# Kernel tuning notes

Hardware: AMD Instinct MI355X
Metric: run time of the kernel (lower is better)

## Reference

```python
import jax, jax.numpy as jnp
import numpy as np

N_NODES = 50000
N_EDGES = 1600000
IN_DIM = 128
HID = 64
N_GRAPHS = 256


def gcn_conv(x, row, col, W, b, n_nodes):
    """PyG GCNConv: symmetric gcn_norm with self-loops, linear-then-aggregate."""
    h = x @ W  # [N, out]
    loop = jnp.arange(n_nodes, dtype=row.dtype)
    r = jnp.concatenate([row, loop])  # sources (messages from x[r])
    c = jnp.concatenate([col, loop])  # targets (aggregate at c)
    ew = jnp.ones(r.shape[0], dtype=x.dtype)
    deg = jax.ops.segment_sum(ew, c, num_segments=n_nodes)
    dinv = jnp.where(deg > 0, jax.lax.rsqrt(deg), 0.0).astype(x.dtype)
    norm = dinv[r] * dinv[c]  # [E+N]
    out = jax.ops.segment_sum(norm[:, None] * h[r], c, num_segments=n_nodes)
    return out + b


def global_mean_pool(x, batch, n_graphs):
    sums = jax.ops.segment_sum(x, batch, num_segments=n_graphs)
    cnt = jax.ops.segment_sum(jnp.ones(x.shape[0], x.dtype), batch, num_segments=n_graphs)
    return sums / jnp.clip(cnt, 1.0)[:, None]


def setup_inputs() -> dict:
    key = jax.random.key(0)
    ks = jax.random.split(key, 12)
    x = jax.random.normal(ks[0], (N_NODES, IN_DIM), dtype=jnp.float32)
    edge_index = jax.random.randint(ks[1], (2, N_EDGES), 0, N_NODES, dtype=jnp.int64)
    batch = jnp.sort(jax.random.randint(ks[2], (N_NODES,), 0, N_GRAPHS, dtype=jnp.int64))
    def glorot(k, shp):
        lim = float(np.sqrt(6.0 / (shp[0] + shp[1])))
        return jax.random.uniform(k, shp, jnp.float32, -lim, lim)
    return {
        "x": x,
        "edge_index": edge_index,
        "batch": batch,
        "W1": glorot(ks[3], (IN_DIM, HID)), "b1": jnp.zeros((HID,), jnp.float32),
        "W2": glorot(ks[4], (HID, HID)), "b2": jnp.zeros((HID,), jnp.float32),
        "W3": glorot(ks[5], (HID, HID)), "b3": jnp.zeros((HID,), jnp.float32),
        "Wl1": glorot(ks[6], (HID, 16)), "bl1": jnp.zeros((16,), jnp.float32),
        "Wl2": glorot(ks[7], (16, 1)), "bl2": jnp.zeros((1,), jnp.float32),
    }


def reference(x, edge_index, batch, W1, b1, W2, b2, W3, b3, Wl1, bl1, Wl2, bl2):
    n = x.shape[0]
    row, col = edge_index[0], edge_index[1]
    h = jax.nn.relu(gcn_conv(x, row, col, W1, b1, n))
    h = jax.nn.relu(gcn_conv(h, row, col, W2, b2, n))
    h = jax.nn.relu(gcn_conv(h, row, col, W3, b3, n))
    g = global_mean_pool(h, batch, N_GRAPHS)  # [G, 64]
    out = (g @ Wl1 + bl1) @ Wl2 + bl2  # [G, 1]
    return out
```

## Files before the change

### kernel.cpp

```cpp
#include <hip/hip_runtime.h>

#define HID 64
#define B1 512
#define NBMAX 200
#define CAP 10368
#define ENTCAP 3456

typedef __attribute__((ext_vector_type(8))) short short8;
typedef __attribute__((ext_vector_type(4))) float float4v;

__device__ __forceinline__ ushort f2bf(float f) {
  unsigned u = __float_as_uint(f);
  unsigned r = (u + 0x7fffu + ((u >> 16) & 1u)) >> 16;
  return (ushort)r;
}
__device__ __forceinline__ float bf2f(ushort v) {
  return __uint_as_float(((unsigned)v) << 16);
}
__device__ __forceinline__ float4 up4(ushort4 v) {
  float4 r;
  r.x = bf2f(v.x);
  r.y = bf2f(v.y);
  r.z = bf2f(v.z);
  r.w = bf2f(v.w);
  return r;
}


__global__ __launch_bounds__(256) void bucket_hist(const int* __restrict__ col, int E, int epb,
                                                   int* __restrict__ blockcnt,
                                                   const float* __restrict__ W1,
                                                   const float* __restrict__ W2,
                                                   const float* __restrict__ W3,
                                                   ushort* __restrict__ Wt1h, ushort* __restrict__ Wt1l,
                                                   ushort* __restrict__ Wt2h, ushort* __restrict__ Wt2l,
                                                   ushort* __restrict__ Wt3h, ushort* __restrict__ Wt3l) {
  int b = blockIdx.x, t = threadIdx.x;
  int gt = b * 256 + t;
  if (gt < 128 * 64) {
    int k = gt >> 6, nn = gt & 63;
    float w = W1[gt];
    ushort h = f2bf(w);
    Wt1h[nn * 128 + k] = h;
    Wt1l[nn * 128 + k] = f2bf(w - bf2f(h));
  }
  if (gt < 64 * 64) {
    int k = gt >> 6, nn = gt & 63;
    float w2 = W2[gt], w3 = W3[gt];
    ushort h2 = f2bf(w2), h3 = f2bf(w3);
    Wt2h[nn * 64 + k] = h2;
    Wt2l[nn * 64 + k] = f2bf(w2 - bf2f(h2));
    Wt3h[nn * 64 + k] = h3;
    Wt3l[nn * 64 + k] = f2bf(w3 - bf2f(h3));
  }

  __shared__ int cnt[256];
  cnt[t] = 0;
  __syncthreads();
  int lo = b * epb, hi = min(lo + epb, E);
  for (int e = lo + t; e < hi; e += 256) atomicAdd(&cnt[col[e] >> 8], 1);
  __syncthreads();
  blockcnt[b * 256 + t] = cnt[t];
}

__global__ __launch_bounds__(512) void scan_blocks(int* __restrict__ blockcnt,
                                                   int* __restrict__ buckettot) {
  __shared__ int s[512];
  int k = blockIdx.x;
  int t = threadIdx.x;
  int v = blockcnt[t * 256 + k];
  s[t] = v;
  __syncthreads();
  for (int d = 1; d < 512; d <<= 1) {
    int u = (t >= d) ? s[t - d] : 0;
    __syncthreads();
    s[t] += u;
    __syncthreads();
  }
  blockcnt[t * 256 + k] = s[t] - v;
  if (t == 511) buckettot[k] = s[t];
}

__global__ __launch_bounds__(256) void scan_buckettot(const int* __restrict__ buckettot,
                                                      int* __restrict__ bucketbase,
                                                      int* __restrict__ csr_off, int n, int E,
                                                      int nb) {
  __shared__ int s[256];
  int t = threadIdx.x;
  int v = buckettot[t];
  s[t] = v;
  __syncthreads();
  for (int d = 1; d < 256; d <<= 1) {
    int u = (t >= d) ? s[t - d] : 0;
    __syncthreads();
    s[t] += u;
    __syncthreads();
  }
  bucketbase[t] = s[t] - v;
  if (t == 255) bucketbase[256] = s[255];
  if (t == 0) csr_off[n] = E;
}

__global__ __launch_bounds__(256) void bin_edges(const int* __restrict__ row,
                                                 const int* __restrict__ col, int E, int epb,
                                                 const int* __restrict__ blockcnt,
                                                 const int* __restrict__ bucketbase,
                                                 unsigned* __restrict__ binned) {
  __shared__ int cnt[256];
  __shared__ int ofs[256];
  __shared__ int gb[256];
  __shared__ int lcur[256];
  __shared__ unsigned ent[ENTCAP];
  __shared__ unsigned stage[ENTCAP];
  int b = blockIdx.x, t = threadIdx.x;
  int lo = b * epb, hi = min(lo + epb, E);
  int ecnt = hi - lo;

  cnt[t] = 0;
  __syncthreads();
  for (int i = t; i < ecnt; i += 256) {
    int c = col[lo + i];
    int r = row[lo + i];
    ent[i] = ((unsigned)r << 16) | (unsigned)c;
    atomicAdd(&cnt[c >> 8], 1);
  }
  __syncthreads();
  int v = cnt[t];
  ofs[t] = v;
  __syncthreads();
  for (int d = 1; d < 256; d <<= 1) {
    int u = (t >= d) ? ofs[t - d] : 0;
    __syncthreads();
    ofs[t] += u;
    __syncthreads();
  }
  int excl = ofs[t] - v;
  int g = bucketbase[t] + blockcnt[b * 256 + t];
  __syncthreads();
  ofs[t] = excl;
  gb[t] = g;
  lcur[t] = excl;
  __syncthreads();
  for (int i = t; i < ecnt; i += 256) {
    unsigned en = ent[i];
    int p = atomicAdd(&lcur[(en >> 8) & 255], 1);
    stage[p] = en;
  }
  __syncthreads();
  for (int i = t; i < ecnt; i += 256) {
    unsigned en = stage[i];
    int bb = (en >> 8) & 255;
    binned[gb[bb] + (i - ofs[bb])] = en;
  }
}

__global__ __launch_bounds__(512) void bucket_csr(const unsigned* __restrict__ binned,
                                                  const int* __restrict__ bucketbase,
                                                  int* __restrict__ csr_off,
                                                  int* __restrict__ csr_src,
                                                  float* __restrict__ dinv, int n) {
  __shared__ int lcnt[256];
  __shared__ int lofs[256];
  __shared__ int lsrc[CAP];
  int k = blockIdx.x, t = threadIdx.x;
  int base = bucketbase[k], end = bucketbase[k + 1];
  int s = end - base;
  if (t < 256) lcnt[t] = 0;
  __syncthreads();
  for (int i = t; i < s; i += 512) {
    unsigned p = binned[base + i];
    atomicAdd(&lcnt[p & 255u], 1);
  }
  __syncthreads();
  int v = 0;
  if (t < 256) {
    v = lcnt[t];
    lofs[t] = v;
  }
  __syncthreads();
  for (int d = 1; d < 256; d <<= 1) {
    int u = (t < 256 && t >= d) ? lofs[t - d] : 0;
    __syncthreads();
    if (t < 256) lofs[t] += u;
    __syncthreads();
  }
  if (t < 256) {
    int excl = lofs[t] - v;
    int node = (k << 8) + t;
    if (node < n) {
      csr_off[node] = base + excl;
      dinv[node] = rsqrtf((float)(v + 1));
    }
    lcnt[t] = excl;
  }
  __syncthreads();
  for (int i = t; i < s; i += 512) {
    unsigned p = binned[base + i];
    int pos = atomicAdd(&lcnt[p & 255u], 1);
    if (pos < CAP) lsrc[pos] = (int)(p >> 16);
  }
  __syncthreads();
  for (int i = t; i < s; i += 512) csr_src[base + i] = (i < CAP) ? lsrc[i] : 0;
}


template <int K>
__global__ __launch_bounds__(256) void gemm_mfma(const float* __restrict__ A,
                                                 const ushort* __restrict__ Wh,
                                                 const ushort* __restrict__ Wl,
                                                 const float* __restrict__ dinv,
                                                 ushort* __restrict__ out, int n) {
  int wave = (blockIdx.x * 256 + threadIdx.x) >> 6;
  int lane = threadIdx.x & 63;
  int row0 = wave * 16;
  if (row0 >= n) return;
  int m = lane & 15;
  int quad = lane >> 4;
  int r = row0 + m;
  int rc = (r < n) ? r : (n - 1);

  float4v acc[4];
#pragma unroll
  for (int t = 0; t < 4; ++t) acc[t] = (float4v){0.f, 0.f, 0.f, 0.f};

#pragma unroll
  for (int k0 = 0; k0 < K; k0 += 32) {
    const float4* xp = (const float4*)&A[(size_t)rc * K + k0 + quad * 8];
    float4 a0 = xp[0];
    float4 a1 = xp[1];
    float av[8] = {a0.x, a0.y, a0.z, a0.w, a1.x, a1.y, a1.z, a1.w};
    short8 ah, al;
#pragma unroll
    for (int i = 0; i < 8; ++i) {
      ushort h = f2bf(av[i]);
      ah[i] = (short)h;
      al[i] = (short)f2bf(av[i] - bf2f(h));
    }
#pragma unroll
    for (int t = 0; t < 4; ++t) {
      size_t wof = (size_t)(t * 16 + m) * K + k0 + quad * 8;
      short8 bh = *(const short8*)&Wh[wof];
      short8 bl = *(const short8*)&Wl[wof];
      acc[t] = __builtin_amdgcn_mfma_f32_16x16x32_bf16(ah, bh, acc[t], 0, 0, 0);
      acc[t] = __builtin_amdgcn_mfma_f32_16x16x32_bf16(al, bh, acc[t], 0, 0, 0);
      acc[t] = __builtin_amdgcn_mfma_f32_16x16x32_bf16(ah, bl, acc[t], 0, 0, 0);
    }
  }

  float4 dv = ((const float4*)dinv)[(row0 >> 2) + quad];
  float dvi[4] = {dv.x, dv.y, dv.z, dv.w};
#pragma unroll
  for (int i = 0; i < 4; ++i) {
    int orow = row0 + quad * 4 + i;
    if (orow < n) {
#pragma unroll
      for (int t = 0; t < 4; ++t) {
        out[(size_t)orow * 64 + t * 16 + m] = f2bf(dvi[i] * acc[t][i]);
      }
    }
  }
}


__global__ __launch_bounds__(256) void agg_kernel(
    const ushort* __restrict__ hs, const int* __restrict__ csr_off,
    const int* __restrict__ csr_src, const float* __restrict__ dinv,
    const float* __restrict__ bias, float* __restrict__ out, int n) {
  int wid = (blockIdx.x * 256 + threadIdx.x) >> 6;
  int lane = threadIdx.x & 63;
  if (wid >= n) return;
  int qe = lane >> 4;
  int fq = lane & 15;
  const ushort4* hs4 = (const ushort4*)hs;

  float4 acc = make_float4(0.f, 0.f, 0.f, 0.f);
  if (qe == 0) {
    float4 s = up4(hs4[(size_t)wid * 16 + fq]);
    acc.x += s.x; acc.y += s.y; acc.z += s.z; acc.w += s.w;
  }

  int j = csr_off[wid];
  int e = csr_off[wid + 1];

  int pre = min(e, (j + 3) & ~3);
  if (j + qe < pre) {
    int s0 = csr_src[j + qe];
    float4 f = up4(hs4[(size_t)s0 * 16 + fq]);
    acc.x += f.x; acc.y += f.y; acc.z += f.z; acc.w += f.w;
  }
  int base = pre;

  for (; base + 16 <= e; base += 16) {
    int4 s = *(const int4*)&csr_src[base + qe * 4];
    float4 f0 = up4(hs4[(size_t)s.x * 16 + fq]);
    float4 f1 = up4(hs4[(size_t)s.y * 16 + fq]);
    float4 f2 = up4(hs4[(size_t)s.z * 16 + fq]);
    float4 f3 = up4(hs4[(size_t)s.w * 16 + fq]);
    acc.x += f0.x + f1.x + f2.x + f3.x;
    acc.y += f0.y + f1.y + f2.y + f3.y;
    acc.z += f0.z + f1.z + f2.z + f3.z;
    acc.w += f0.w + f1.w + f2.w + f3.w;
  }

  for (; base + 4 <= e; base += 4) {
    int s0 = csr_src[base + qe];
    float4 f = up4(hs4[(size_t)s0 * 16 + fq]);
    acc.x += f.x; acc.y += f.y; acc.z += f.z; acc.w += f.w;
  }
  if (base + qe < e) {
    int s0 = csr_src[base + qe];
    float4 f = up4(hs4[(size_t)s0 * 16 + fq]);
    acc.x += f.x; acc.y += f.y; acc.z += f.z; acc.w += f.w;
  }

  acc.x += __shfl_xor(acc.x, 16, 64);
  acc.y += __shfl_xor(acc.y, 16, 64);
  acc.z += __shfl_xor(acc.z, 16, 64);
  acc.w += __shfl_xor(acc.w, 16, 64);
  acc.x += __shfl_xor(acc.x, 32, 64);
  acc.y += __shfl_xor(acc.y, 32, 64);
  acc.z += __shfl_xor(acc.z, 32, 64);
  acc.w += __shfl_xor(acc.w, 32, 64);

  if (qe == 0) {
    float d = dinv[wid];
    float4 bi = ((const float4*)bias)[fq];
    float4 r;
    r.x = fmaxf(d * acc.x + bi.x, 0.f);
    r.y = fmaxf(d * acc.y + bi.y, 0.f);
    r.z = fmaxf(d * acc.z + bi.z, 0.f);
    r.w = fmaxf(d * acc.w + bi.w, 0.f);
    ((float4*)out)[(size_t)wid * 16 + fq] = r;
  }
}


__global__ __launch_bounds__(256) void pool_mlp_kernel(
    const float* __restrict__ a, const int* __restrict__ batch, int n,
    const float* __restrict__ Wl1, const float* __restrict__ bl1,
    const float* __restrict__ Wl2, const float* __restrict__ bl2,
    float* __restrict__ out) {
  int g = blockIdx.x;
  int t = threadIdx.x;
  int lane = t & 63;
  int w = t >> 6;

  int lo = 0, hi = n;
  while (lo < hi) {
    int m = (lo + hi) >> 1;
    if (batch[m] < g) lo = m + 1; else hi = m;
  }
  int start = lo;
  lo = start; hi = n;
  while (lo < hi) {
    int m = (lo + hi) >> 1;
    if (batch[m] < g + 1) lo = m + 1; else hi = m;
  }
  int end = lo;

  float s = 0.f;
  for (int i = start + w; i < end; i += 4) s += a[i * 64 + lane];

  __shared__ float ps[4][64];
  __shared__ float gv[64];
  __shared__ float hv[16];
  ps[w][lane] = s;
  __syncthreads();
  if (w == 0) {
    float tot = ps[0][lane] + ps[1][lane] + ps[2][lane] + ps[3][lane];
    gv[lane] = tot / (float)max(end - start, 1);
  }
  __syncthreads();
  if (t < 16) {
    float h = bl1[t];
    for (int k = 0; k < 64; ++k) h += gv[k] * Wl1[k * 16 + t];
    hv[t] = h;
  }
  __syncthreads();
  if (t == 0) {
    float o = bl2[0];
    for (int j2 = 0; j2 < 16; ++j2) o += hv[j2] * Wl2[j2];
    out[g] = o;
  }
}


extern "C" void kernel_launch(void* const* d_in, const int* in_sizes, int n_in,
                              void* d_out, int out_size, void* d_ws, size_t ws_size,
                              hipStream_t stream) {
  const float* x = (const float*)d_in[0];
  const int* ei = (const int*)d_in[1];
  const int* batch = (const int*)d_in[2];
  const float* W1 = (const float*)d_in[3];
  const float* b1 = (const float*)d_in[4];
  const float* W2 = (const float*)d_in[5];
  const float* b2 = (const float*)d_in[6];
  const float* W3 = (const float*)d_in[7];
  const float* b3 = (const float*)d_in[8];
  const float* Wl1 = (const float*)d_in[9];
  const float* bl1 = (const float*)d_in[10];
  const float* Wl2 = (const float*)d_in[11];
  const float* bl2 = (const float*)d_in[12];

  int n = in_sizes[0] / 128;
  int E = in_sizes[1] / 2;
  int G = out_size;
  int nb = (n + 255) >> 8;
  int epb = (E + B1 - 1) / B1;

  const int* row = ei;
  const int* col = ei + E;

  char* p = (char*)d_ws;
  int* blockcnt = (int*)p;    p += B1 * 256 * 4;
  int* buckettot = (int*)p;   p += 256 * 4;
  int* bucketbase = (int*)p;  p += 272 * 4;
  int* csr_off = (int*)p;     p += 50064 * 4;
  float* dinv = (float*)p;    p += 50016 * 4;
  ushort* Wt1h = (ushort*)p;  p += 128 * 64 * 2;
  ushort* Wt1l = (ushort*)p;  p += 128 * 64 * 2;
  ushort* Wt2h = (ushort*)p;  p += 64 * 64 * 2;
  ushort* Wt2l = (ushort*)p;  p += 64 * 64 * 2;
  ushort* Wt3h = (ushort*)p;  p += 64 * 64 * 2;
  ushort* Wt3l = (ushort*)p;  p += 64 * 64 * 2;
  int* csr_src = (int*)p;     p += (size_t)((E + 15) / 16 * 16) * 4;
  ushort* hs = (ushort*)p;    p += (size_t)n * 64 * 2;
  float* abuf = (float*)p;
  unsigned* binned = (unsigned*)hs;

  bucket_hist<<<B1, 256, 0, stream>>>(col, E, epb, blockcnt,
                                      W1, W2, W3, Wt1h, Wt1l, Wt2h, Wt2l, Wt3h, Wt3l);
  scan_blocks<<<256, 512, 0, stream>>>(blockcnt, buckettot);
  scan_buckettot<<<1, 256, 0, stream>>>(buckettot, bucketbase, csr_off, n, E, nb);
  bin_edges<<<B1, 256, 0, stream>>>(row, col, E, epb, blockcnt, bucketbase, binned);
  bucket_csr<<<nb, 512, 0, stream>>>(binned, bucketbase, csr_off, csr_src, dinv, n);

  int nwaves = (n + 15) / 16;
  int gblocks = (nwaves + 3) / 4;
  int ablocks = (n * 64 + 255) / 256;

  gemm_mfma<128><<<gblocks, 256, 0, stream>>>(x, Wt1h, Wt1l, dinv, hs, n);
  agg_kernel<<<ablocks, 256, 0, stream>>>(hs, csr_off, csr_src, dinv, b1, abuf, n);
  gemm_mfma<64><<<gblocks, 256, 0, stream>>>(abuf, Wt2h, Wt2l, dinv, hs, n);
  agg_kernel<<<ablocks, 256, 0, stream>>>(hs, csr_off, csr_src, dinv, b2, abuf, n);
  gemm_mfma<64><<<gblocks, 256, 0, stream>>>(abuf, Wt3h, Wt3l, dinv, hs, n);
  agg_kernel<<<ablocks, 256, 0, stream>>>(hs, csr_off, csr_src, dinv, b3, abuf, n);
  pool_mlp_kernel<<<G, 256, 0, stream>>>(abuf, batch, n, Wl1, bl1, Wl2, bl2, (float*)d_out);
}
```

Measured before the change: 309.5 us.

## Vectorize edge loads, cache binned entries in registers, pack bf16 accumulation

The histogram and binning kernels now read col/row as int4 vectors, with epb rounded up to a multiple of 16 so each block's start stays aligned. bucket_csr keeps each thread's binned entries in a fixed register array so the second pass skips the global re-read. The aggregation kernel unpacks bf16 pairs with shifts and masks into packed float2 accumulators instead of four scalar converts. ENTCAP shrinks to match the new per-block edge count. The cost removed is extra global traffic and conversion ALU work, at the price of more registers and a hard cap of 21 entries per thread in bucket_csr; entries past that limit are never read, so correctness now depends on bucket sizes staying within the cap.

Result: no change. 306.9 us (-0.8%).

```diff
diff --git a/kernel.cpp b/kernel.cpp
--- a/kernel.cpp
+++ b/kernel.cpp
@@ -4,10 +4,12 @@
 #define B1 512
 #define NBMAX 200
 #define CAP 10368
-#define ENTCAP 3456
+#define ENTCAP 3200
+#define CPT 21
 
 typedef __attribute__((ext_vector_type(8))) short short8;
 typedef __attribute__((ext_vector_type(4))) float float4v;
+typedef float f32x2 __attribute__((ext_vector_type(2)));
 
 __device__ __forceinline__ ushort f2bf(float f) {
   unsigned u = __float_as_uint(f);
@@ -17,13 +19,15 @@
 __device__ __forceinline__ float bf2f(ushort v) {
   return __uint_as_float(((unsigned)v) << 16);
 }
-__device__ __forceinline__ float4 up4(ushort4 v) {
-  float4 r;
-  r.x = bf2f(v.x);
-  r.y = bf2f(v.y);
-  r.z = bf2f(v.z);
-  r.w = bf2f(v.w);
-  return r;
+
+__device__ __forceinline__ void acc8(f32x2& a01, f32x2& a23, uint2 d) {
+  f32x2 t0, t1;
+  t0.x = __uint_as_float(d.x << 16);
+  t0.y = __uint_as_float(d.x & 0xffff0000u);
+  t1.x = __uint_as_float(d.y << 16);
+  t1.y = __uint_as_float(d.y & 0xffff0000u);
+  a01 += t0;
+  a23 += t1;
 }
 
 
@@ -58,7 +62,18 @@
   cnt[t] = 0;
   __syncthreads();
   int lo = b * epb, hi = min(lo + epb, E);
-  for (int e = lo + t; e < hi; e += 256) atomicAdd(&cnt[col[e] >> 8], 1);
+  int ecnt = hi - lo;
+  if (ecnt > 0) {
+    int ecnt4 = ecnt & ~3;
+    for (int i = t * 4; i < ecnt4; i += 1024) {
+      int4 c4 = *(const int4*)&col[lo + i];
+      atomicAdd(&cnt[c4.x >> 8], 1);
+      atomicAdd(&cnt[c4.y >> 8], 1);
+      atomicAdd(&cnt[c4.z >> 8], 1);
+      atomicAdd(&cnt[c4.w >> 8], 1);
+    }
+    for (int i = ecnt4 + t; i < ecnt; i += 256) atomicAdd(&cnt[col[lo + i] >> 8], 1);
+  }
   __syncthreads();
   blockcnt[b * 256 + t] = cnt[t];
 }
@@ -118,11 +133,28 @@
 
   cnt[t] = 0;
   __syncthreads();
-  for (int i = t; i < ecnt; i += 256) {
-    int c = col[lo + i];
-    int r = row[lo + i];
-    ent[i] = ((unsigned)r << 16) | (unsigned)c;
-    atomicAdd(&cnt[c >> 8], 1);
+  if (ecnt > 0) {
+    int ecnt4 = ecnt & ~3;
+    for (int i = t * 4; i < ecnt4; i += 1024) {
+      int4 c4 = *(const int4*)&col[lo + i];
+      int4 r4 = *(const int4*)&row[lo + i];
+      uint4 e4;
+      e4.x = ((unsigned)r4.x << 16) | (unsigned)c4.x;
+      e4.y = ((unsigned)r4.y << 16) | (unsigned)c4.y;
+      e4.z = ((unsigned)r4.z << 16) | (unsigned)c4.z;
+      e4.w = ((unsigned)r4.w << 16) | (unsigned)c4.w;
+      *(uint4*)&ent[i] = e4;
+      atomicAdd(&cnt[c4.x >> 8], 1);
+      atomicAdd(&cnt[c4.y >> 8], 1);
+      atomicAdd(&cnt[c4.z >> 8], 1);
+      atomicAdd(&cnt[c4.w >> 8], 1);
+    }
+    for (int i = ecnt4 + t; i < ecnt; i += 256) {
+      int c = col[lo + i];
+      int r = row[lo + i];
+      ent[i] = ((unsigned)r << 16) | (unsigned)c;
+      atomicAdd(&cnt[c >> 8], 1);
+    }
   }
   __syncthreads();
   int v = cnt[t];
@@ -141,16 +173,20 @@
   gb[t] = g;
   lcur[t] = excl;
   __syncthreads();
-  for (int i = t; i < ecnt; i += 256) {
-    unsigned en = ent[i];
-    int p = atomicAdd(&lcur[(en >> 8) & 255], 1);
-    stage[p] = en;
-  }
-  __syncthreads();
-  for (int i = t; i < ecnt; i += 256) {
-    unsigned en = stage[i];
-    int bb = (en >> 8) & 255;
-    binned[gb[bb] + (i - ofs[bb])] = en;
+  if (ecnt > 0) {
+    for (int i = t; i < ecnt; i += 256) {
+      unsigned en = ent[i];
+      int p = atomicAdd(&lcur[(en >> 8) & 255], 1);
+      stage[p] = en;
+    }
+  }
+  __syncthreads();
+  if (ecnt > 0) {
+    for (int i = t; i < ecnt; i += 256) {
+      unsigned en = stage[i];
+      int bb = (en >> 8) & 255;
+      binned[gb[bb] + (i - ofs[bb])] = en;
+    }
   }
 }
 
@@ -165,11 +201,17 @@
   int k = blockIdx.x, t = threadIdx.x;
   int base = bucketbase[k], end = bucketbase[k + 1];
   int s = end - base;
+  unsigned ent[CPT];
   if (t < 256) lcnt[t] = 0;
   __syncthreads();
-  for (int i = t; i < s; i += 512) {
-    unsigned p = binned[base + i];
-    atomicAdd(&lcnt[p & 255u], 1);
+#pragma unroll
+  for (int q = 0; q < CPT; ++q) {
+    int i = q * 512 + t;
+    if (i < s) {
+      unsigned p = binned[base + i];
+      ent[q] = p;
+      atomicAdd(&lcnt[p & 255u], 1);
+    }
   }
   __syncthreads();
   int v = 0;
@@ -194,10 +236,14 @@
     lcnt[t] = excl;
   }
   __syncthreads();
-  for (int i = t; i < s; i += 512) {
-    unsigned p = binned[base + i];
-    int pos = atomicAdd(&lcnt[p & 255u], 1);
-    if (pos < CAP) lsrc[pos] = (int)(p >> 16);
+#pragma unroll
+  for (int q = 0; q < CPT; ++q) {
+    int i = q * 512 + t;
+    if (i < s) {
+      unsigned p = ent[q];
+      int pos = atomicAdd(&lcnt[p & 255u], 1);
+      if (pos < CAP) lsrc[pos] = (int)(p >> 16);
+    }
   }
   __syncthreads();
   for (int i = t; i < s; i += 512) csr_src[base + i] = (i < CAP) ? lsrc[i] : 0;
@@ -271,12 +317,11 @@
   if (wid >= n) return;
   int qe = lane >> 4;
   int fq = lane & 15;
-  const ushort4* hs4 = (const ushort4*)hs;
-
-  float4 acc = make_float4(0.f, 0.f, 0.f, 0.f);
+  const uint2* hs2 = (const uint2*)hs;
+
+  f32x2 a01 = {0.f, 0.f}, a23 = {0.f, 0.f};
   if (qe == 0) {
-    float4 s = up4(hs4[(size_t)wid * 16 + fq]);
-    acc.x += s.x; acc.y += s.y; acc.z += s.z; acc.w += s.w;
+    acc8(a01, a23, hs2[(size_t)wid * 16 + fq]);
   }
 
   int j = csr_off[wid];
@@ -285,51 +330,48 @@
   int pre = min(e, (j + 3) & ~3);
   if (j + qe < pre) {
     int s0 = csr_src[j + qe];
-    float4 f = up4(hs4[(size_t)s0 * 16 + fq]);
-    acc.x += f.x; acc.y += f.y; acc.z += f.z; acc.w += f.w;
+    acc8(a01, a23, hs2[(size_t)s0 * 16 + fq]);
   }
   int base = pre;
 
   for (; base + 16 <= e; base += 16) {
     int4 s = *(const int4*)&csr_src[base + qe * 4];
-    float4 f0 = up4(hs4[(size_t)s.x * 16 + fq]);
-    float4 f1 = up4(hs4[(size_t)s.y * 16 + fq]);
-    float4 f2 = up4(hs4[(size_t)s.z * 16 + fq]);
-    float4 f3 = up4(hs4[(size_t)s.w * 16 + fq]);
-    acc.x += f0.x + f1.x + f2.x + f3.x;
-    acc.y += f0.y + f1.y + f2.y + f3.y;
-    acc.z += f0.z + f1.z + f2.z + f3.z;
-    acc.w += f0.w + f1.w + f2.w + f3.w;
+    uint2 v0 = hs2[(size_t)s.x * 16 + fq];
+    uint2 v1 = hs2[(size_t)s.y * 16 + fq];
+    uint2 v2 = hs2[(size_t)s.z * 16 + fq];
+    uint2 v3 = hs2[(size_t)s.w * 16 + fq];
+    acc8(a01, a23, v0);
+    acc8(a01, a23, v1);
+    acc8(a01, a23, v2);
+    acc8(a01, a23, v3);
   }
 
   for (; base + 4 <= e; base += 4) {
     int s0 = csr_src[base + qe];
-    float4 f = up4(hs4[(size_t)s0 * 16 + fq]);
-    acc.x += f.x; acc.y += f.y; acc.z += f.z; acc.w += f.w;
+    acc8(a01, a23, hs2[(size_t)s0 * 16 + fq]);
   }
   if (base + qe < e) {
     int s0 = csr_src[base + qe];
-    float4 f = up4(hs4[(size_t)s0 * 16 + fq]);
-    acc.x += f.x; acc.y += f.y; acc.z += f.z; acc.w += f.w;
-  }
-
-  acc.x += __shfl_xor(acc.x, 16, 64);
-  acc.y += __shfl_xor(acc.y, 16, 64);
-  acc.z += __shfl_xor(acc.z, 16, 64);
-  acc.w += __shfl_xor(acc.w, 16, 64);
-  acc.x += __shfl_xor(acc.x, 32, 64);
-  acc.y += __shfl_xor(acc.y, 32, 64);
-  acc.z += __shfl_xor(acc.z, 32, 64);
-  acc.w += __shfl_xor(acc.w, 32, 64);
+    acc8(a01, a23, hs2[(size_t)s0 * 16 + fq]);
+  }
+
+  a01.x += __shfl_xor(a01.x, 16, 64);
+  a01.y += __shfl_xor(a01.y, 16, 64);
+  a23.x += __shfl_xor(a23.x, 16, 64);
+  a23.y += __shfl_xor(a23.y, 16, 64);
+  a01.x += __shfl_xor(a01.x, 32, 64);
+  a01.y += __shfl_xor(a01.y, 32, 64);
+  a23.x += __shfl_xor(a23.x, 32, 64);
+  a23.y += __shfl_xor(a23.y, 32, 64);
 
   if (qe == 0) {
     float d = dinv[wid];
     float4 bi = ((const float4*)bias)[fq];
     float4 r;
-    r.x = fmaxf(d * acc.x + bi.x, 0.f);
-    r.y = fmaxf(d * acc.y + bi.y, 0.f);
-    r.z = fmaxf(d * acc.z + bi.z, 0.f);
-    r.w = fmaxf(d * acc.w + bi.w, 0.f);
+    r.x = fmaxf(d * a01.x + bi.x, 0.f);
+    r.y = fmaxf(d * a01.y + bi.y, 0.f);
+    r.z = fmaxf(d * a23.x + bi.z, 0.f);
+    r.w = fmaxf(d * a23.y + bi.w, 0.f);
     ((float4*)out)[(size_t)wid * 16 + fq] = r;
   }
 }
@@ -406,7 +448,7 @@
   int E = in_sizes[1] / 2;
   int G = out_size;
   int nb = (n + 255) >> 8;
-  int epb = (E + B1 - 1) / B1;
+  int epb = (((E + B1 - 1) / B1) + 15) & ~15;
 
   const int* row = ei;
   const int* col = ei + E;
```
